# Optimization experiments

Measured on AMD Instinct MI355X. Metric: run time of the kernel, lower is better.

Reference implementation:

```python
import jax, jax.numpy as jnp
import numpy as np

# --- fixed model configuration (from init_kwargs) ---
NX, NY, NU, NP = 8, 8, 2, 5
DELTA = 0.01
PHO, CP, AR, AB = 5.0, 6.0, 3.0, 3.0
KR, KB, TD, QR, QB = 2.5, 1.5, 300.0, 200.0, 200.0
CAF, TF = 6.0, 320.0
YMEAN = jnp.array([50.0, 1.0, 0.5, 313.0, 50.0, 1.0, 0.5, 313.0], jnp.float32)
YSTD = jnp.array([2.0, 0.2, 0.1, 4.0, 2.0, 0.2, 0.1, 4.0], jnp.float32)
UMEAN = jnp.array([10.0, 5.0], jnp.float32)
USTD = jnp.array([1.0, 0.5], jnp.float32)


def _fg(x, u):
    """Grey-box CSTR+flash ODE RHS. x: [B,8] scaled, u: [B,2] scaled."""
    x = x * YSTD + YMEAN
    u = u * USTD + UMEAN
    Hr, CAr, CBr, Tr = x[..., 0:1], x[..., 1:2], x[..., 2:3], x[..., 3:4]
    Hb, CAb, CBb, Tb = x[..., 4:5], x[..., 5:6], x[..., 6:7], x[..., 7:8]
    F, D = u[..., 0:1], u[..., 1:2]
    Fr = KR * jnp.sqrt(Hr)
    Fb = KB * jnp.sqrt(Hb)
    dHr = (F + D - Fr) / AR
    dCAr = (F * (CAF - CAr) - D * CAr) / (AR * Hr)
    dCBr = (-F * CBr - D * CBr) / (AR * Hr)
    dTr = (F * (TF - Tr) + D * (TD - Tr)) / (AR * Hr) + QR / (PHO * AR * CP * Hr)
    dHb = (Fr - Fb - D) / AB
    dCAb = (Fr * (CAr - CAb) + D * CAb) / (AB * Hb)
    dCBb = (Fr * (CBr - CBb) + D * CBb) / (AB * Hb)
    dTb = Fr * (Tr - Tb) / (AB * Hb) + QB / (PHO * AB * CP * Hb)
    xdot = jnp.concatenate([dHr, dCAr, dCBr, dTr, dHb, dCAb, dCBb, dTb], axis=-1)
    return xdot / YSTD


def setup_inputs() -> dict:
    key = jax.random.key(0)
    ks = jax.random.split(key, 6)
    B, T = 2048, 128
    d_in, d_h = NX + NP * (NY + NU) + NU, 128  # 60, 128
    useq = jax.random.normal(ks[0], (B, T, NU), jnp.float32)
    xGz0 = jax.random.normal(ks[1], (B, NX + NP * (NY + NU)), jnp.float32)
    W1 = jax.random.normal(ks[2], (d_in, d_h), jnp.float32) * (1.0 / np.sqrt(d_in))
    b1 = jnp.zeros((d_h,), jnp.float32)
    W2 = jax.random.normal(ks[3], (d_h, d_h), jnp.float32) * (1.0 / np.sqrt(d_h))
    b2 = jnp.zeros((d_h,), jnp.float32)
    W3 = jax.random.normal(ks[4], (d_h, NX), jnp.float32) * (1.0 / np.sqrt(d_h))
    b3 = jnp.zeros((NX,), jnp.float32)
    return {"useq": useq, "xGz0": xGz0, "W1": W1, "b1": b1,
            "W2": W2, "b2": b2, "W3": W3, "b3": b3}


def reference(useq, xGz0, W1, b1, W2, b2, W3, b3):
    def fnn(inp):
        h = jnp.tanh(inp @ W1 + b1)
        h = jnp.tanh(h @ W2 + b2)
        return h @ W3 + b3

    def interp(yfull):  # [B,(Np+1)*Ny] -> [B,Np*Ny]
        B = yfull.shape[0]
        y = yfull.reshape(B, NP + 1, NY)
        return (0.5 * (y[:, :-1] + y[:, 1:])).reshape(B, NP * NY)

    def step(xGz, u):
        xG = xGz[:, :NX]
        z = xGz[:, NX:]
        ypseq = z[:, :NP * NY]
        upseq = z[:, NP * NY:]
        # k1
        k1 = _fg(xG, u) + fnn(jnp.concatenate((xG, z, u), axis=-1))
        # interpolated half-step past sequence
        yp_interp = interp(jnp.concatenate((ypseq, xG), axis=-1))
        z_half = jnp.concatenate((yp_interp, upseq), axis=-1)
        x2 = xG + DELTA * (k1 / 2)
        k2 = _fg(x2, u) + fnn(jnp.concatenate((x2, z_half, u), axis=-1))
        x3 = xG + DELTA * (k2 / 2)
        k3 = _fg(x3, u) + fnn(jnp.concatenate((x3, z_half, u), axis=-1))
        yp_shift = jnp.concatenate((ypseq[:, NY:], xG), axis=-1)
        z_full = jnp.concatenate((yp_shift, upseq), axis=-1)
        x4 = xG + DELTA * k3
        k4 = _fg(x4, u) + fnn(jnp.concatenate((x4, z_full, u), axis=-1))
        y = xG
        xGplus = xG + (DELTA / 6) * (k1 + 2 * k2 + 2 * k3 + k4)
        zplus = jnp.concatenate((yp_shift, upseq[:, NU:], u), axis=-1)
        return jnp.concatenate((xGplus, zplus), axis=-1), y

    u_t = jnp.swapaxes(useq, 0, 1)  # [T,B,Nu]
    _, ys = jax.lax.scan(step, xGz0, u_t)  # ys: [T,B,Ny]
    return jnp.swapaxes(ys, 0, 1)  # [B,T,Ny]
```

## Files before the change

kernel.cpp:

```cpp
#include <hip/hip_runtime.h>
#include <math.h>

#define BLOCK 512
#define ROWS 8

typedef __attribute__((ext_vector_type(8))) short s16x8;
typedef __attribute__((ext_vector_type(4))) float f32x4;

static constexpr int O_H1   = 0;
static constexpr int O_SU   = 1088;
static constexpr int O_PP   = 3168;
static constexpr int O_PRIV = 3680;
static constexpr int PRIV_DW = 640;
static constexpr int LDSN   = O_PRIV + 8 * PRIV_DW;

static constexpr float SCL = 2.88539008177792681f;

__device__ __forceinline__ unsigned short f2bf(float f) {
  unsigned u = __float_as_uint(f);
  return (unsigned short)((u + 0x7fffu + ((u >> 16) & 1u)) >> 16);
}
__device__ __forceinline__ unsigned cvt_pk_bf16(float lo, float hi) {
  unsigned r;
  asm("v_cvt_pk_bf16_f32 %0, %1, %2" : "=v"(r) : "v"(lo), "v"(hi));
  return r;
}
__device__ __forceinline__ unsigned short bf1(float v) {
  return (unsigned short)cvt_pk_bf16(v, v);
}
__device__ __forceinline__ float tanh_ps(float y) {
  float e = __builtin_amdgcn_exp2f(y);
  return fmaf(-2.f, __builtin_amdgcn_rcpf(e + 1.f), 1.f);
}

#define MFMA16(A, B, C) __builtin_amdgcn_mfma_f32_16x16x32_bf16((A), (B), (C), 0, 0, 0)

extern "C" __global__ void __launch_bounds__(BLOCK, 1)
cstr_rk4_mfma10(const float* __restrict__ useq, const float* __restrict__ xGz0,
                const float* __restrict__ W1, const float* __restrict__ b1,
                const float* __restrict__ W2, const float* __restrict__ b2,
                const float* __restrict__ W3, const float* __restrict__ b3,
                float* __restrict__ out)
{
  extern __shared__ float smf[];
  unsigned short* h1h = (unsigned short*)(smf + O_H1);
  unsigned*       h1u = (unsigned*)(smf + O_H1);
  float* su = smf + O_SU;
  float* pp = smf + O_PP;

  const int tid  = threadIdx.x;
  const int w    = tid >> 6;
  const int l    = tid & 63;
  const int nn   = l & 15;
  const int hh   = l >> 4;
  const int r    = l >> 3;
  const int c    = l & 7;
  const int base = blockIdx.x * ROWS;

  float* wp_ = smf + O_PRIV + w * PRIV_DW;
  unsigned short* inhp = (unsigned short*)wp_;
  float* xmp = wp_ + 576;

  for (int i = tid; i < 8 * 260; i += BLOCK) {
    int row = i / 260, col = i % 260;
    su[i] = (col < 256) ? useq[(size_t)base * 256 + row * 256 + col] : 0.f;
  }
  for (int i = l; i < 16 * 72; i += 64) {
    int n_ = i / 72, k = i % 72;
    unsigned short v = 0;
    if (n_ < ROWS) {
      if (k < 58)      v = f2bf(xGz0[(size_t)(base + n_) * 58 + k]);
      else if (k < 60) v = f2bf(useq[(size_t)(base + n_) * 256 + (k - 58)]);
    }
    inhp[i] = v;
  }
  xmp[l] = xGz0[(size_t)(base + r) * 58 + c];

  const size_t rowb = (size_t)(base + r) * 58;
  float xg  = xGz0[rowb + c];
  float yp0 = xGz0[rowb + 8 + c],  yp1 = xGz0[rowb + 16 + c];
  float yp2 = xGz0[rowb + 24 + c], yp3 = xGz0[rowb + 32 + c];
  float yp4 = xGz0[rowb + 40 + c];
  float upA = xGz0[rowb + 48 + c];
  float upB = (c < 2) ? xGz0[rowb + 56 + c] : 0.f;
  float b3r = b3[c];
  float kacc = 0.f;

  const int j = 16 * w + nn;
  s16x8 a10, a11, a20, a21, a22, a23, a3h;
  #pragma unroll
  for (int i = 0; i < 8; ++i) {
    int k0 = 8 * hh + i, k1 = 32 + 8 * hh + i;
    a10[i] = (short)f2bf(SCL * W1[k0 * 128 + j]);
    a11[i] = (short)((k1 < 60) ? f2bf(SCL * W1[k1 * 128 + j]) : 0);
    a20[i] = (short)f2bf(SCL * W2[(     8 * hh + i) * 128 + j]);
    a21[i] = (short)f2bf(SCL * W2[(32 + 8 * hh + i) * 128 + j]);
    a22[i] = (short)f2bf(SCL * W2[(64 + 8 * hh + i) * 128 + j]);
    a23[i] = (short)f2bf(SCL * W2[(96 + 8 * hh + i) * 128 + j]);
    unsigned short z = 0;
    if (i < 4 && nn < 8) z = f2bf(W3[(16 * w + 4 * hh + i) * 8 + nn]);
    a3h[i] = (short)z;
  }
  const float4 bt1 = *(const float4*)(b1 + 16 * w + 4 * hh);
  const float4 bt2 = *(const float4*)(b2 + 16 * w + 4 * hh);
  const f32x4 cinit1 = {SCL * bt1.x, SCL * bt1.y, SCL * bt1.z, SCL * bt1.w};
  const f32x4 cinit2 = {SCL * bt2.x, SCL * bt2.y, SCL * bt2.z, SCL * bt2.w};
  const f32x4 zf = {0.f, 0.f, 0.f, 0.f};

  __syncthreads();

  #pragma unroll 1
  for (int t = 0; t < 128; ++t) {
    const float u0r = su[r * 260 + 2 * t];
    const float u1r = su[r * 260 + 2 * t + 1];
    if (w == 0) out[((size_t)(base + r) * 128 + t) * 8 + c] = xg;

    #pragma unroll
    for (int s = 0; s < 4; ++s) {
      {
        s16x8 bb0 = *(const s16x8*)(inhp + nn * 72 + 8 * hh);
        s16x8 bb1 = *(const s16x8*)(inhp + nn * 72 + 32 + 8 * hh);
        f32x4 c1a = MFMA16(a10, bb0, cinit1);
        f32x4 c1b = MFMA16(a11, bb1, zf);
        f32x4 c1 = c1a + c1b;
        float t0 = tanh_ps(c1[0]);
        float t1 = tanh_ps(c1[1]);
        float t2 = tanh_ps(c1[2]);
        float t3 = tanh_ps(c1[3]);
        uint2 pk; pk.x = cvt_pk_bf16(t0, t1); pk.y = cvt_pk_bf16(t2, t3);
        *(uint2*)(h1u + nn * 68 + 8 * w + 2 * hh) = pk;
      }
      __syncthreads();

      {
        const unsigned short* h1row = h1h + nn * 136;
        s16x8 q0 = *(const s16x8*)(h1row +  0 + 8 * hh);
        s16x8 q1 = *(const s16x8*)(h1row + 32 + 8 * hh);
        s16x8 q2 = *(const s16x8*)(h1row + 64 + 8 * hh);
        s16x8 q3 = *(const s16x8*)(h1row + 96 + 8 * hh);
        f32x4 c2a = MFMA16(a20, q0, cinit2);
        f32x4 c2b = MFMA16(a21, q1, zf);
        c2a = MFMA16(a22, q2, c2a);
        c2b = MFMA16(a23, q3, c2b);
        f32x4 c2 = c2a + c2b;
        float t0 = tanh_ps(c2[0]);
        float t1 = tanh_ps(c2[1]);
        float t2 = tanh_ps(c2[2]);
        float t3 = tanh_ps(c2[3]);
        s16x8 bf3;
        ((unsigned*)&bf3)[0] = cvt_pk_bf16(t0, t1);
        ((unsigned*)&bf3)[1] = cvt_pk_bf16(t2, t3);
        ((unsigned*)&bf3)[2] = 0u;
        ((unsigned*)&bf3)[3] = 0u;
        f32x4 c3p = MFMA16(a3h, bf3, zf);
        if (nn < 8 && hh < 2)
          *(float4*)(pp + w * 64 + nn * 8 + 4 * hh) =
              make_float4(c3p[0], c3p[1], c3p[2], c3p[3]);
      }
      __syncthreads();

      {
        float nv = b3r;
        #pragma unroll
        for (int ww = 0; ww < 8; ++ww) nv += pp[ww * 64 + l];
        float4 xa = *(const float4*)(xmp + r * 8);
        float4 xb = *(const float4*)(xmp + r * 8 + 4);
        float Hr  = fmaf(xa.x, 2.f, 50.f),  CAr = fmaf(xa.y, 0.2f, 1.f);
        float CBr = fmaf(xa.z, 0.1f, 0.5f), Tr  = fmaf(xa.w, 4.f, 313.f);
        float Hb  = fmaf(xb.x, 2.f, 50.f),  CAb = fmaf(xb.y, 0.2f, 1.f);
        float CBb = fmaf(xb.z, 0.1f, 0.5f), Tb  = fmaf(xb.w, 4.f, 313.f);
        float F = u0r + 10.f, D = fmaf(u1r, 0.5f, 5.f);
        float Fr = 2.5f * sqrtf(Hr), Fb = 1.5f * sqrtf(Hb);
        float rH = __builtin_amdgcn_rcpf(3.f * Hr);
        float rB = __builtin_amdgcn_rcpf(3.f * Hb);
        float k0 = (F + D - Fr) * (1.f / 6.f);
        float k1 = (F * (6.f - CAr) - D * CAr) * (5.f * rH);
        float k2 = (-(F + D) * CBr) * (10.f * rH);
        float k3 = (F * (320.f - Tr) + D * (300.f - Tr)) * (0.25f * rH) + (5.f / 3.f) * rH;
        float k4 = (Fr - Fb - D) * (1.f / 6.f);
        float k5 = (Fr * (CAr - CAb) + D * CAb) * (5.f * rB);
        float k6 = (Fr * (CBr - CBb) + D * CBb) * (10.f * rB);
        float k7 = Fr * (Tr - Tb) * (0.25f * rB) + (5.f / 3.f) * rB;
        float fgc = (c & 4) ? ((c & 2) ? ((c & 1) ? k7 : k6) : ((c & 1) ? k5 : k4))
                            : ((c & 2) ? ((c & 1) ? k3 : k2) : ((c & 1) ? k1 : k0));
        float kv = fgc + nv;
        float cc;
        if (s == 0)      { kacc = kv;                  cc = fmaf(kv, 0.005f, xg); }
        else if (s == 1) { kacc = fmaf(kv, 2.f, kacc); cc = fmaf(kv, 0.005f, xg); }
        else if (s == 2) { kacc = fmaf(kv, 2.f, kacc); cc = fmaf(kv, 0.01f,  xg); }
        else             { xg = fmaf(kacc + kv, 0.01f / 6.f, xg); cc = xg; }
        xmp[r * 8 + c] = cc;
        inhp[r * 72 + c] = bf1(cc);

        if (s == 0) {
          inhp[r * 72 +  8 + c] = bf1(0.5f * (yp0 + yp1));
          inhp[r * 72 + 16 + c] = bf1(0.5f * (yp1 + yp2));
          inhp[r * 72 + 24 + c] = bf1(0.5f * (yp2 + yp3));
          inhp[r * 72 + 32 + c] = bf1(0.5f * (yp3 + yp4));
          inhp[r * 72 + 40 + c] = bf1(0.5f * (yp4 + xg));
        } else if (s == 2) {
          inhp[r * 72 +  8 + c] = bf1(yp1);
          inhp[r * 72 + 16 + c] = bf1(yp2);
          inhp[r * 72 + 24 + c] = bf1(yp3);
          inhp[r * 72 + 32 + c] = bf1(yp4);
          inhp[r * 72 + 40 + c] = bf1(xg);
          yp0 = yp1; yp1 = yp2; yp2 = yp3; yp3 = yp4; yp4 = xg;
        } else if (s == 3) {
          float tA = __shfl(upA, (l & 56) + ((c + 2) & 7));
          float tB = __shfl(upB, (l & 56) + ((c >= 6) ? (c - 6) : 0));
          float nu = (c < 6) ? tA : tB;
          upA = nu;
          inhp[r * 72 + 48 + c] = bf1(nu);
          if (c < 2) {
            float uv = (c == 0) ? u0r : u1r;
            upB = uv;
            inhp[r * 72 + 56 + c] = bf1(uv);
            if (t < 127)
              inhp[r * 72 + 58 + c] = bf1(su[r * 260 + 2 * (t + 1) + c]);
          }
        }
      }
    }
  }
}

extern "C" void kernel_launch(void* const* d_in, const int* in_sizes, int n_in,
                              void* d_out, int out_size, void* d_ws, size_t ws_size,
                              hipStream_t stream) {
  const float* useq = (const float*)d_in[0];
  const float* xGz0 = (const float*)d_in[1];
  const float* W1   = (const float*)d_in[2];
  const float* b1   = (const float*)d_in[3];
  const float* W2   = (const float*)d_in[4];
  const float* b2   = (const float*)d_in[5];
  const float* W3   = (const float*)d_in[6];
  const float* b3   = (const float*)d_in[7];
  float* out = (float*)d_out;

  size_t lds = (size_t)LDSN * sizeof(float);
  (void)hipFuncSetAttribute((const void*)cstr_rk4_mfma10,
                            hipFuncAttributeMaxDynamicSharedMemorySize, (int)lds);
  hipLaunchKernelGGL(cstr_rk4_mfma10, dim3(2048 / ROWS), dim3(BLOCK), lds, stream,
                     useq, xGz0, W1, b1, W2, b2, W3, b3, out);
}
```

Baseline: 492.9 us.

## Collapse 8-wave block into single wave holding all weights in registers

Each block now runs as one 64-lane wave instead of eight waves. That wave keeps all eight 16-column weight tiles in registers and runs every layer's MFMAs itself. This removes the two block-wide barriers per RK stage and the LDS partial-sum reduction for layer 3; the layer-3 result is now gathered across lanes with shuffles. The trade-off is a much larger register footprint per wave, which risks spills. It also serialises the MFMA and tanh work onto one wave, and the s-loop is no longer unrolled.

```diff
diff --git a/kernel.cpp b/kernel.cpp
--- a/kernel.cpp
+++ b/kernel.cpp
@@ -1,18 +1,17 @@
 #include <hip/hip_runtime.h>
 #include <math.h>
 
-#define BLOCK 512
+#define BLOCK 64
 #define ROWS 8
 
 typedef __attribute__((ext_vector_type(8))) short s16x8;
 typedef __attribute__((ext_vector_type(4))) float f32x4;
 
-static constexpr int O_H1   = 0;
-static constexpr int O_SU   = 1088;
-static constexpr int O_PP   = 3168;
-static constexpr int O_PRIV = 3680;
-static constexpr int PRIV_DW = 640;
-static constexpr int LDSN   = O_PRIV + 8 * PRIV_DW;
+static constexpr int O_H1  = 0;
+static constexpr int O_INH = 1088;
+static constexpr int O_XM  = 1664;
+static constexpr int O_SU  = 1728;
+static constexpr int LDSN  = 3808;
 
 static constexpr float SCL = 2.88539008177792681f;
 
@@ -36,32 +35,27 @@
 #define MFMA16(A, B, C) __builtin_amdgcn_mfma_f32_16x16x32_bf16((A), (B), (C), 0, 0, 0)
 
 extern "C" __global__ void __launch_bounds__(BLOCK, 1)
-cstr_rk4_mfma10(const float* __restrict__ useq, const float* __restrict__ xGz0,
-                const float* __restrict__ W1, const float* __restrict__ b1,
-                const float* __restrict__ W2, const float* __restrict__ b2,
-                const float* __restrict__ W3, const float* __restrict__ b3,
-                float* __restrict__ out)
+cstr_rk4_sw(const float* __restrict__ useq, const float* __restrict__ xGz0,
+            const float* __restrict__ W1, const float* __restrict__ b1,
+            const float* __restrict__ W2, const float* __restrict__ b2,
+            const float* __restrict__ W3, const float* __restrict__ b3,
+            float* __restrict__ out)
 {
   extern __shared__ float smf[];
   unsigned short* h1h = (unsigned short*)(smf + O_H1);
   unsigned*       h1u = (unsigned*)(smf + O_H1);
+  unsigned short* inh = (unsigned short*)(smf + O_INH);
+  float* xm = smf + O_XM;
   float* su = smf + O_SU;
-  float* pp = smf + O_PP;
-
-  const int tid  = threadIdx.x;
-  const int w    = tid >> 6;
-  const int l    = tid & 63;
-  const int nn   = l & 15;
-  const int hh   = l >> 4;
-  const int r    = l >> 3;
-  const int c    = l & 7;
+
+  const int l  = threadIdx.x;
+  const int nn = l & 15;
+  const int hh = l >> 4;
+  const int r  = l >> 3;
+  const int c  = l & 7;
   const int base = blockIdx.x * ROWS;
 
-  float* wp_ = smf + O_PRIV + w * PRIV_DW;
-  unsigned short* inhp = (unsigned short*)wp_;
-  float* xmp = wp_ + 576;
-
-  for (int i = tid; i < 8 * 260; i += BLOCK) {
+  for (int i = l; i < 8 * 260; i += 64) {
     int row = i / 260, col = i % 260;
     su[i] = (col < 256) ? useq[(size_t)base * 256 + row * 256 + col] : 0.f;
   }
@@ -72,9 +66,9 @@
       if (k < 58)      v = f2bf(xGz0[(size_t)(base + n_) * 58 + k]);
       else if (k < 60) v = f2bf(useq[(size_t)(base + n_) * 256 + (k - 58)]);
     }
-    inhp[i] = v;
-  }
-  xmp[l] = xGz0[(size_t)(base + r) * 58 + c];
+    inh[i] = v;
+  }
+  xm[l] = xGz0[(size_t)(base + r) * 58 + c];
 
   const size_t rowb = (size_t)(base + r) * 58;
   float xg  = xGz0[rowb + c];
@@ -86,85 +80,84 @@
   float b3r = b3[c];
   float kacc = 0.f;
 
-  const int j = 16 * w + nn;
-  s16x8 a10, a11, a20, a21, a22, a23, a3h;
+  s16x8 a1x[8][2], a2x[8][4], a3x[8];
+  f32x4 ci1[8], ci2[8];
   #pragma unroll
-  for (int i = 0; i < 8; ++i) {
-    int k0 = 8 * hh + i, k1 = 32 + 8 * hh + i;
-    a10[i] = (short)f2bf(SCL * W1[k0 * 128 + j]);
-    a11[i] = (short)((k1 < 60) ? f2bf(SCL * W1[k1 * 128 + j]) : 0);
-    a20[i] = (short)f2bf(SCL * W2[(     8 * hh + i) * 128 + j]);
-    a21[i] = (short)f2bf(SCL * W2[(32 + 8 * hh + i) * 128 + j]);
-    a22[i] = (short)f2bf(SCL * W2[(64 + 8 * hh + i) * 128 + j]);
-    a23[i] = (short)f2bf(SCL * W2[(96 + 8 * hh + i) * 128 + j]);
-    unsigned short z = 0;
-    if (i < 4 && nn < 8) z = f2bf(W3[(16 * w + 4 * hh + i) * 8 + nn]);
-    a3h[i] = (short)z;
-  }
-  const float4 bt1 = *(const float4*)(b1 + 16 * w + 4 * hh);
-  const float4 bt2 = *(const float4*)(b2 + 16 * w + 4 * hh);
-  const f32x4 cinit1 = {SCL * bt1.x, SCL * bt1.y, SCL * bt1.z, SCL * bt1.w};
-  const f32x4 cinit2 = {SCL * bt2.x, SCL * bt2.y, SCL * bt2.z, SCL * bt2.w};
+  for (int m = 0; m < 8; ++m) {
+    const int j = 16 * m + nn;
+    #pragma unroll
+    for (int i = 0; i < 8; ++i) {
+      const int k0 = 8 * hh + i, k1 = 32 + 8 * hh + i;
+      a1x[m][0][i] = (short)f2bf(SCL * W1[k0 * 128 + j]);
+      a1x[m][1][i] = (short)((k1 < 60) ? f2bf(SCL * W1[k1 * 128 + j]) : 0);
+      #pragma unroll
+      for (int p = 0; p < 4; ++p)
+        a2x[m][p][i] = (short)f2bf(SCL * W2[(32 * p + 8 * hh + i) * 128 + j]);
+      unsigned short z = 0;
+      if (i < 4 && nn < 8) z = f2bf(W3[(16 * m + 4 * hh + i) * 8 + nn]);
+      a3x[m][i] = (short)z;
+    }
+    const float4 bt1 = *(const float4*)(b1 + 16 * m + 4 * hh);
+    const float4 bt2 = *(const float4*)(b2 + 16 * m + 4 * hh);
+    ci1[m] = (f32x4){SCL * bt1.x, SCL * bt1.y, SCL * bt1.z, SCL * bt1.w};
+    ci2[m] = (f32x4){SCL * bt2.x, SCL * bt2.y, SCL * bt2.z, SCL * bt2.w};
+  }
   const f32x4 zf = {0.f, 0.f, 0.f, 0.f};
-
-  __syncthreads();
+  const int srcl = ((c >> 2) << 4) + r;
 
   #pragma unroll 1
   for (int t = 0; t < 128; ++t) {
     const float u0r = su[r * 260 + 2 * t];
     const float u1r = su[r * 260 + 2 * t + 1];
-    if (w == 0) out[((size_t)(base + r) * 128 + t) * 8 + c] = xg;
-
-    #pragma unroll
+    out[((size_t)(base + r) * 128 + t) * 8 + c] = xg;
+
+    #pragma unroll 1
     for (int s = 0; s < 4; ++s) {
-      {
-        s16x8 bb0 = *(const s16x8*)(inhp + nn * 72 + 8 * hh);
-        s16x8 bb1 = *(const s16x8*)(inhp + nn * 72 + 32 + 8 * hh);
-        f32x4 c1a = MFMA16(a10, bb0, cinit1);
-        f32x4 c1b = MFMA16(a11, bb1, zf);
-        f32x4 c1 = c1a + c1b;
-        float t0 = tanh_ps(c1[0]);
-        float t1 = tanh_ps(c1[1]);
-        float t2 = tanh_ps(c1[2]);
-        float t3 = tanh_ps(c1[3]);
-        uint2 pk; pk.x = cvt_pk_bf16(t0, t1); pk.y = cvt_pk_bf16(t2, t3);
-        *(uint2*)(h1u + nn * 68 + 8 * w + 2 * hh) = pk;
+      s16x8 bb0 = *(const s16x8*)(inh + nn * 72 + 8 * hh);
+      s16x8 bb1 = *(const s16x8*)(inh + nn * 72 + 32 + 8 * hh);
+      float4 xa = *(const float4*)(xm + r * 8);
+      float4 xb = *(const float4*)(xm + r * 8 + 4);
+      #pragma unroll
+      for (int m = 0; m < 8; ++m) {
+        f32x4 c1 = MFMA16(a1x[m][0], bb0, ci1[m]);
+        c1 = MFMA16(a1x[m][1], bb1, c1);
+        uint2 pk;
+        pk.x = cvt_pk_bf16(tanh_ps(c1[0]), tanh_ps(c1[1]));
+        pk.y = cvt_pk_bf16(tanh_ps(c1[2]), tanh_ps(c1[3]));
+        *(uint2*)(h1u + nn * 68 + 8 * m + 2 * hh) = pk;
       }
-      __syncthreads();
-
-      {
-        const unsigned short* h1row = h1h + nn * 136;
-        s16x8 q0 = *(const s16x8*)(h1row +  0 + 8 * hh);
-        s16x8 q1 = *(const s16x8*)(h1row + 32 + 8 * hh);
-        s16x8 q2 = *(const s16x8*)(h1row + 64 + 8 * hh);
-        s16x8 q3 = *(const s16x8*)(h1row + 96 + 8 * hh);
-        f32x4 c2a = MFMA16(a20, q0, cinit2);
-        f32x4 c2b = MFMA16(a21, q1, zf);
-        c2a = MFMA16(a22, q2, c2a);
-        c2b = MFMA16(a23, q3, c2b);
+
+      const unsigned short* h1row = h1h + nn * 136;
+      s16x8 q0 = *(const s16x8*)(h1row +  0 + 8 * hh);
+      s16x8 q1 = *(const s16x8*)(h1row + 32 + 8 * hh);
+      s16x8 q2 = *(const s16x8*)(h1row + 64 + 8 * hh);
+      s16x8 q3 = *(const s16x8*)(h1row + 96 + 8 * hh);
+      f32x4 c3a = zf, c3b = zf;
+      #pragma unroll
+      for (int m = 0; m < 8; ++m) {
+        f32x4 c2a = MFMA16(a2x[m][0], q0, ci2[m]);
+        f32x4 c2b = MFMA16(a2x[m][1], q1, zf);
+        c2a = MFMA16(a2x[m][2], q2, c2a);
+        c2b = MFMA16(a2x[m][3], q3, c2b);
         f32x4 c2 = c2a + c2b;
-        float t0 = tanh_ps(c2[0]);
-        float t1 = tanh_ps(c2[1]);
-        float t2 = tanh_ps(c2[2]);
-        float t3 = tanh_ps(c2[3]);
         s16x8 bf3;
-        ((unsigned*)&bf3)[0] = cvt_pk_bf16(t0, t1);
-        ((unsigned*)&bf3)[1] = cvt_pk_bf16(t2, t3);
+        ((unsigned*)&bf3)[0] = cvt_pk_bf16(tanh_ps(c2[0]), tanh_ps(c2[1]));
+        ((unsigned*)&bf3)[1] = cvt_pk_bf16(tanh_ps(c2[2]), tanh_ps(c2[3]));
         ((unsigned*)&bf3)[2] = 0u;
         ((unsigned*)&bf3)[3] = 0u;
-        f32x4 c3p = MFMA16(a3h, bf3, zf);
-        if (nn < 8 && hh < 2)
-          *(float4*)(pp + w * 64 + nn * 8 + 4 * hh) =
-              make_float4(c3p[0], c3p[1], c3p[2], c3p[3]);
+        if (m & 1) c3b = MFMA16(a3x[m], bf3, c3b);
+        else       c3a = MFMA16(a3x[m], bf3, c3a);
       }
-      __syncthreads();
+      f32x4 c3p = c3a + c3b;
 
       {
-        float nv = b3r;
-        #pragma unroll
-        for (int ww = 0; ww < 8; ++ww) nv += pp[ww * 64 + l];
-        float4 xa = *(const float4*)(xmp + r * 8);
-        float4 xb = *(const float4*)(xmp + r * 8 + 4);
+        float v0 = __shfl(c3p[0], srcl);
+        float v1 = __shfl(c3p[1], srcl);
+        float v2 = __shfl(c3p[2], srcl);
+        float v3 = __shfl(c3p[3], srcl);
+        float nv = b3r + ((c & 2) ? ((c & 1) ? v3 : v2)
+                                  : ((c & 1) ? v1 : v0));
+
         float Hr  = fmaf(xa.x, 2.f, 50.f),  CAr = fmaf(xa.y, 0.2f, 1.f);
         float CBr = fmaf(xa.z, 0.1f, 0.5f), Tr  = fmaf(xa.w, 4.f, 313.f);
         float Hb  = fmaf(xb.x, 2.f, 50.f),  CAb = fmaf(xb.y, 0.2f, 1.f);
@@ -189,34 +182,34 @@
         else if (s == 1) { kacc = fmaf(kv, 2.f, kacc); cc = fmaf(kv, 0.005f, xg); }
         else if (s == 2) { kacc = fmaf(kv, 2.f, kacc); cc = fmaf(kv, 0.01f,  xg); }
         else             { xg = fmaf(kacc + kv, 0.01f / 6.f, xg); cc = xg; }
-        xmp[r * 8 + c] = cc;
-        inhp[r * 72 + c] = bf1(cc);
+        xm[r * 8 + c] = cc;
+        inh[r * 72 + c] = bf1(cc);
 
         if (s == 0) {
-          inhp[r * 72 +  8 + c] = bf1(0.5f * (yp0 + yp1));
-          inhp[r * 72 + 16 + c] = bf1(0.5f * (yp1 + yp2));
-          inhp[r * 72 + 24 + c] = bf1(0.5f * (yp2 + yp3));
-          inhp[r * 72 + 32 + c] = bf1(0.5f * (yp3 + yp4));
-          inhp[r * 72 + 40 + c] = bf1(0.5f * (yp4 + xg));
+          inh[r * 72 +  8 + c] = bf1(0.5f * (yp0 + yp1));
+          inh[r * 72 + 16 + c] = bf1(0.5f * (yp1 + yp2));
+          inh[r * 72 + 24 + c] = bf1(0.5f * (yp2 + yp3));
+          inh[r * 72 + 32 + c] = bf1(0.5f * (yp3 + yp4));
+          inh[r * 72 + 40 + c] = bf1(0.5f * (yp4 + xg));
         } else if (s == 2) {
-          inhp[r * 72 +  8 + c] = bf1(yp1);
-          inhp[r * 72 + 16 + c] = bf1(yp2);
-          inhp[r * 72 + 24 + c] = bf1(yp3);
-          inhp[r * 72 + 32 + c] = bf1(yp4);
-          inhp[r * 72 + 40 + c] = bf1(xg);
+          inh[r * 72 +  8 + c] = bf1(yp1);
+          inh[r * 72 + 16 + c] = bf1(yp2);
+          inh[r * 72 + 24 + c] = bf1(yp3);
+          inh[r * 72 + 32 + c] = bf1(yp4);
+          inh[r * 72 + 40 + c] = bf1(xg);
           yp0 = yp1; yp1 = yp2; yp2 = yp3; yp3 = yp4; yp4 = xg;
         } else if (s == 3) {
           float tA = __shfl(upA, (l & 56) + ((c + 2) & 7));
           float tB = __shfl(upB, (l & 56) + ((c >= 6) ? (c - 6) : 0));
           float nu = (c < 6) ? tA : tB;
           upA = nu;
-          inhp[r * 72 + 48 + c] = bf1(nu);
+          inh[r * 72 + 48 + c] = bf1(nu);
           if (c < 2) {
             float uv = (c == 0) ? u0r : u1r;
             upB = uv;
-            inhp[r * 72 + 56 + c] = bf1(uv);
+            inh[r * 72 + 56 + c] = bf1(uv);
             if (t < 127)
-              inhp[r * 72 + 58 + c] = bf1(su[r * 260 + 2 * (t + 1) + c]);
+              inh[r * 72 + 58 + c] = bf1(su[r * 260 + 2 * (t + 1) + c]);
           }
         }
       }
@@ -238,8 +231,8 @@
   float* out = (float*)d_out;
 
   size_t lds = (size_t)LDSN * sizeof(float);
-  (void)hipFuncSetAttribute((const void*)cstr_rk4_mfma10,
+  (void)hipFuncSetAttribute((const void*)cstr_rk4_sw,
                             hipFuncAttributeMaxDynamicSharedMemorySize, (int)lds);
-  hipLaunchKernelGGL(cstr_rk4_mfma10, dim3(2048 / ROWS), dim3(BLOCK), lds, stream,
+  hipLaunchKernelGGL(cstr_rk4_sw, dim3(2048 / ROWS), dim3(BLOCK), lds, stream,
                      useq, xGz0, W1, b1, W2, b2, W3, b3, out);
 }
```

Result: slower. 1.022 ms (+107.4%).
